# Kernel optimization log

Measured on AMD Instinct MI355X. Metric: run time of the kernel, lower is better.

## Reference

```python
import jax, jax.numpy as jnp
import numpy as np

B, N, C, P, K = 8, 65536, 96, 96, 512


def _ln(x, g, b, eps=1e-5):
    mu = x.mean(axis=-1, keepdims=True)
    var = ((x - mu) ** 2).mean(axis=-1, keepdims=True)
    return (x - mu) * jax.lax.rsqrt(var + eps) * g + b


def setup_inputs():
    key = jax.random.key(0)
    ks = jax.random.split(key, 8)
    inp = {
        "pts_feat": jax.random.normal(ks[0], (B, N, C), jnp.float32),
        "sp_idx": jax.random.randint(ks[1], (B, N), 0, K, jnp.int64),
        "all_xyz": jax.random.normal(ks[2], (B, N, 3), jnp.float32),
        # pts_proj1: Linear(3,P) -> LN -> ReLU -> Linear(P,P) -> LN
        "W1": jax.random.normal(ks[3], (3, P), jnp.float32) / np.sqrt(3.0),
        "b1": jnp.zeros((P,), jnp.float32),
        "g1": jnp.ones((P,), jnp.float32),
        "be1": jnp.zeros((P,), jnp.float32),
        "W2": jax.random.normal(ks[4], (P, P), jnp.float32) / np.sqrt(P),
        "b2": jnp.zeros((P,), jnp.float32),
        "g2": jnp.ones((P,), jnp.float32),
        "be2": jnp.zeros((P,), jnp.float32),
        # pts_proj2: Linear(2P,P) -> LN -> ReLU -> Linear(P,1,no bias) -> Sigmoid
        "W3": jax.random.normal(ks[5], (2 * P, P), jnp.float32) / np.sqrt(2.0 * P),
        "b3": jnp.zeros((P,), jnp.float32),
        "g3": jnp.ones((P,), jnp.float32),
        "be3": jnp.zeros((P,), jnp.float32),
        "W4": jax.random.normal(ks[6], (P, 1), jnp.float32) / np.sqrt(P),
        "num_sp": K,
    }
    return inp


def reference(pts_feat, sp_idx, all_xyz, W1, b1, g1, be1, W2, b2, g2, be2,
              W3, b3, g3, be3, W4, num_sp):
    Bx, Nx, Cx = pts_feat.shape
    S = Bx * num_sp  # total superpoints across batch (uniform K per batch)
    idx = (sp_idx + jnp.arange(Bx, dtype=sp_idx.dtype)[:, None] * num_sp).reshape(-1)
    xyz = all_xyz.reshape(-1, 3)
    feat = pts_feat.reshape(-1, Cx)

    # scatter_norm: unit-sphere normalize per segment
    mn = jax.ops.segment_min(xyz, idx, num_segments=S)
    mx = jax.ops.segment_max(xyz, idx, num_segments=S)
    cnt = jax.ops.segment_sum(jnp.ones((xyz.shape[0],), xyz.dtype), idx, num_segments=S)
    cnt_c = jnp.maximum(cnt, 1.0)
    center = jax.ops.segment_sum(xyz, idx, num_segments=S) / cnt_c[:, None]
    diam = (mx - mn).max(axis=1)
    pts = (xyz - center[idx]) / (diam[idx][:, None] + 0.01)

    # pts_proj1
    h = _ln(pts @ W1 + b1, g1, be1)
    h = jax.nn.relu(h)
    h = _ln(h @ W2 + b2, g2, be2)

    seg = jax.ops.segment_max(h, idx, num_segments=S)  # (S, P)
    cat = jnp.concatenate([h, seg[idx]], axis=-1)      # (B*N, 2P)

    # pts_proj2
    z = _ln(cat @ W3 + b3, g3, be3)
    z = jax.nn.relu(z)
    w = jax.nn.sigmoid(z @ W4) * 2.0                   # (B*N, 1)

    sp_feat = jax.ops.segment_sum(feat * w, idx, num_segments=S) / cnt_c[:, None] + seg
    return sp_feat.reshape(Bx, num_sp, Cx), w.reshape(Bx, Nx, 1)
```

## Files before the change

kernel.cpp:

```cpp
#include <hip/hip_runtime.h>
#include <cstdint>

#define MM 524288
#define NSEG 4096

#define WS_SCNT   0u
#define WS_CURSOR 4096u
#define WS_OFFS   8192u
#define WS_M1     12288u
#define WS_CENTER 12304u
#define WS_DIAM   24592u
#define WS_SEGF   28688u
#define WS_ZSEG   421904u
#define WS_SORTED 815120u
#define WS_SEG16  1339408u
#define WS_WSRT   1601552u
#define WS_H8     2125840u
#define WS_END    (WS_H8 + 25165824u)

typedef __attribute__((ext_vector_type(8))) short short8;
typedef __attribute__((ext_vector_type(4))) float f32x4;

#define WPAD 104

__device__ __forceinline__ unsigned bfr(float x) {
    unsigned u = __float_as_uint(x);
    return (u + 0x7FFFu + ((u >> 16) & 1u)) >> 16;
}
__device__ __forceinline__ float bf2f(unsigned v) {
    return __uint_as_float(v << 16);
}
union U4S8 { uint4 u; short8 s; };

__global__ void __launch_bounds__(256) k0_init(unsigned* __restrict__ ws)
{
    unsigned i = blockIdx.x * 256u + threadIdx.x;
    if (i < 8192u) ws[i] = 0u;
}

__global__ void __launch_bounds__(256) k1_count(
    const int* __restrict__ spidx, unsigned* __restrict__ scnt)
{
    __shared__ unsigned lcnt[512];
    int tid = threadIdx.x;
    for (int j = tid; j < 512; j += 256) lcnt[j] = 0u;
    __syncthreads();
    int base = blockIdx.x * 4096;
    #pragma unroll 4
    for (int it = 0; it < 16; ++it) {
        int p = base + it*256 + tid;
        atomicAdd(&lcnt[spidx[p]], 1u);
    }
    __syncthreads();
    int b = blockIdx.x >> 4;
    for (int j = tid; j < 512; j += 256)
        atomicAdd(&scnt[(b << 9) + j], lcnt[j]);
}

__global__ void __launch_bounds__(1024) k2_scan(
    const unsigned* __restrict__ scnt, unsigned* __restrict__ offs,
    const float* __restrict__ W1, const float* __restrict__ b1, float* __restrict__ m1)
{
    __shared__ unsigned sh[1024];
    int t = threadIdx.x;
    unsigned c0 = scnt[t*4+0], c1 = scnt[t*4+1], c2 = scnt[t*4+2], c3 = scnt[t*4+3];
    unsigned tot = c0 + c1 + c2 + c3;
    sh[t] = tot;
    __syncthreads();
    for (int d = 1; d < 1024; d <<= 1) {
        unsigned v = (t >= d) ? sh[t-d] : 0u;
        __syncthreads();
        sh[t] += v;
        __syncthreads();
    }
    unsigned excl = sh[t] - tot;
    offs[t*4+0] = excl;
    offs[t*4+1] = excl + c0;
    offs[t*4+2] = excl + c0 + c1;
    offs[t*4+3] = excl + c0 + c1 + c2;

    if (t == 0) {
        float Sa=0,Sb=0,Sc=0,Sd=0,Saa=0,Sbb=0,Scc=0,Sdd=0,Sab=0,Sac=0,Sad=0,Sbc=0,Sbd=0,Scd=0;
        #pragma unroll 8
        for (int j = 0; j < 96; ++j) {
            float A = W1[j], B2 = W1[96+j], C2 = W1[192+j], D = b1[j];
            Sa+=A; Sb+=B2; Sc+=C2; Sd+=D;
            Saa=fmaf(A,A,Saa); Sbb=fmaf(B2,B2,Sbb); Scc=fmaf(C2,C2,Scc); Sdd=fmaf(D,D,Sdd);
            Sab=fmaf(A,B2,Sab); Sac=fmaf(A,C2,Sac); Sad=fmaf(A,D,Sad);
            Sbc=fmaf(B2,C2,Sbc); Sbd=fmaf(B2,D,Sbd); Scd=fmaf(C2,D,Scd);
        }
        const float inv = 1.f/96.f;
        float Am=Sa*inv, Bm=Sb*inv, Cm=Sc*inv, Dm=Sd*inv;
        m1[0]=Am; m1[1]=Bm; m1[2]=Cm; m1[3]=Dm;
        m1[4]=Saa*inv-Am*Am; m1[5]=Sbb*inv-Bm*Bm; m1[6]=Scc*inv-Cm*Cm; m1[7]=Sdd*inv-Dm*Dm;
        m1[8]=Sab*inv-Am*Bm; m1[9]=Sac*inv-Am*Cm; m1[10]=Sad*inv-Am*Dm;
        m1[11]=Sbc*inv-Bm*Cm; m1[12]=Sbd*inv-Bm*Dm; m1[13]=Scd*inv-Cm*Dm;
    }
}

__global__ void __launch_bounds__(256) k3_scatter(
    const int* __restrict__ spidx, const unsigned* __restrict__ offs,
    unsigned* __restrict__ cursor, unsigned* __restrict__ sorted,
    unsigned short* __restrict__ seg16)
{
    __shared__ unsigned lcnt[512];
    __shared__ unsigned gbase[512];
    __shared__ unsigned short rank16[4096];
    int tid = threadIdx.x;
    for (int j = tid; j < 512; j += 256) lcnt[j] = 0u;
    __syncthreads();
    int base = blockIdx.x * 4096;
    #pragma unroll 4
    for (int it = 0; it < 16; ++it) {
        int p = base + it*256 + tid;
        unsigned r = atomicAdd(&lcnt[spidx[p]], 1u);
        rank16[it*256 + tid] = (unsigned short)r;
    }
    __syncthreads();
    int b = blockIdx.x >> 4;
    for (int j = tid; j < 512; j += 256)
        gbase[j] = atomicAdd(&cursor[(b << 9) + j], lcnt[j]);
    __syncthreads();
    #pragma unroll 4
    for (int it = 0; it < 16; ++it) {
        int p = base + it*256 + tid;
        int sl = spidx[p];
        int s = (b << 9) + sl;
        unsigned pos = offs[s] + gbase[sl] + (unsigned)rank16[it*256 + tid];
        sorted[pos] = (unsigned)p;
        seg16[pos] = (unsigned short)s;
    }
}

__global__ void __launch_bounds__(128) k3b_stats(
    const float* __restrict__ xyz, const unsigned* __restrict__ sorted,
    const unsigned* __restrict__ offs, const unsigned* __restrict__ scnt,
    float* __restrict__ center, float* __restrict__ diam)
{
    int s = blockIdx.x, tid = threadIdx.x;
    unsigned cnt = scnt[s], off = offs[s];
    float mnx=INFINITY, mny=INFINITY, mnz=INFINITY;
    float mxx=-INFINITY, mxy=-INFINITY, mxz=-INFINITY;
    float smx=0.f, smy=0.f, smz=0.f;
    for (unsigned r = tid; r < cnt; r += 128) {
        unsigned p = sorted[off + r];
        float x = xyz[3*p], y = xyz[3*p+1], z = xyz[3*p+2];
        mnx = fminf(mnx, x); mny = fminf(mny, y); mnz = fminf(mnz, z);
        mxx = fmaxf(mxx, x); mxy = fmaxf(mxy, y); mxz = fmaxf(mxz, z);
        smx += x; smy += y; smz += z;
    }
    #pragma unroll
    for (int m = 1; m < 64; m <<= 1) {
        mnx = fminf(mnx, __shfl_xor(mnx, m)); mny = fminf(mny, __shfl_xor(mny, m));
        mnz = fminf(mnz, __shfl_xor(mnz, m));
        mxx = fmaxf(mxx, __shfl_xor(mxx, m)); mxy = fmaxf(mxy, __shfl_xor(mxy, m));
        mxz = fmaxf(mxz, __shfl_xor(mxz, m));
        smx += __shfl_xor(smx, m); smy += __shfl_xor(smy, m); smz += __shfl_xor(smz, m);
    }
    __shared__ float cw[2][9];
    if ((tid & 63) == 0) {
        int w = tid >> 6;
        cw[w][0]=mnx; cw[w][1]=mny; cw[w][2]=mnz;
        cw[w][3]=mxx; cw[w][4]=mxy; cw[w][5]=mxz;
        cw[w][6]=smx; cw[w][7]=smy; cw[w][8]=smz;
    }
    __syncthreads();
    if (tid == 0) {
        float a0=fminf(cw[0][0],cw[1][0]), a1=fminf(cw[0][1],cw[1][1]), a2=fminf(cw[0][2],cw[1][2]);
        float b0=fmaxf(cw[0][3],cw[1][3]), b1=fmaxf(cw[0][4],cw[1][4]), b2=fmaxf(cw[0][5],cw[1][5]);
        float s0=cw[0][6]+cw[1][6], s1=cw[0][7]+cw[1][7], s2=cw[0][8]+cw[1][8];
        float cc = fmaxf((float)cnt, 1.f);
        center[s*3+0] = s0/cc; center[s*3+1] = s1/cc; center[s*3+2] = s2/cc;
        diam[s] = fmaxf(fmaxf(b0-a0, b1-a1), b2-a2);
    }
}

__global__ void __launch_bounds__(256) kTA(
    const float* __restrict__ xyz,
    const unsigned* __restrict__ sorted,
    const unsigned short* __restrict__ seg16,
    const float* __restrict__ center, const float* __restrict__ diam,
    const float* __restrict__ W1, const float* __restrict__ b1,
    const float* __restrict__ g1, const float* __restrict__ be1,
    const float* __restrict__ m1,
    const float* __restrict__ W2, const float* __restrict__ b2,
    const float* __restrict__ g2, const float* __restrict__ be2,
    uint4* __restrict__ h8)
{
    __shared__ unsigned short wT[96*WPAD];
    __shared__ float pw8[96*8];
    __shared__ float prm[3*96];
    __shared__ float mcl[14];
    int tid = threadIdx.x;
    #pragma unroll 4
    for (int it = 0; it < 36; ++it) {
        int e = it*256 + tid;
        int i = e / 96, j = e - i*96;
        wT[j*WPAD + i] = (unsigned short)bfr(W2[e]);
    }
    if (tid < 96) {
        pw8[tid*8+0] = W1[tid]; pw8[tid*8+1] = W1[96+tid]; pw8[tid*8+2] = W1[192+tid];
        pw8[tid*8+3] = b1[tid]; pw8[tid*8+4] = g1[tid];    pw8[tid*8+5] = be1[tid];
        pw8[tid*8+6] = 0.f;     pw8[tid*8+7] = 0.f;
        prm[tid] = b2[tid]; prm[96+tid] = g2[tid]; prm[192+tid] = be2[tid];
    }
    if (tid < 14) mcl[tid] = m1[tid];
    __syncthreads();

    int lane = tid & 63, w = tid >> 6;
    int pcol = lane & 15, g = lane >> 4;
    size_t slot0 = (size_t)blockIdx.x * 256 + w*64 + pcol;
    const f32x4* pwv = (const f32x4*)pw8;

    #pragma unroll 1
    for (int t = 0; t < 4; ++t) {
        size_t slot = slot0 + (size_t)t * 16;
        unsigned p = sorted[slot];
        int s = seg16[slot];
        float dinv = 1.f / (diam[s] + 0.01f);
        float px = (xyz[3*p+0] - center[3*s+0]) * dinv;
        float py = (xyz[3*p+1] - center[3*s+1]) * dinv;
        float pz = (xyz[3*p+2] - center[3*s+2]) * dinv;

        float mu = fmaf(px, mcl[0], fmaf(py, mcl[1], fmaf(pz, mcl[2], mcl[3])));
        float var = fmaf(px*px, mcl[4], fmaf(py*py, mcl[5], fmaf(pz*pz, mcl[6], mcl[7])));
        var = fmaf(2.f*px*py, mcl[8],  var);
        var = fmaf(2.f*px*pz, mcl[9],  var);
        var = fmaf(2.f*px,    mcl[10], var);
        var = fmaf(2.f*py*pz, mcl[11], var);
        var = fmaf(2.f*py,    mcl[12], var);
        var = fmaf(2.f*pz,    mcl[13], var);
        float rs = rsqrtf(var + 1e-5f);

        f32x4 acc[6];
        #pragma unroll
        for (int nt = 0; nt < 6; ++nt) acc[nt] = (f32x4){0.f,0.f,0.f,0.f};

        #pragma unroll
        for (int ks = 0; ks < 3; ++ks) {
            U4S8 bu;
            unsigned vv[4];
            #pragma unroll
            for (int e2 = 0; e2 < 4; ++e2) {
                int i0 = ks*32 + g*8 + e2*2;
                f32x4 lo0 = pwv[i0*2],     hi0 = pwv[i0*2+1];
                f32x4 lo1 = pwv[(i0+1)*2], hi1 = pwv[(i0+1)*2+1];
                float ta = fmaf(px, lo0[0], fmaf(py, lo0[1], fmaf(pz, lo0[2], lo0[3])));
                ta = fmaxf(fmaf((ta - mu) * rs, hi0[0], hi0[1]), 0.f);
                float tb = fmaf(px, lo1[0], fmaf(py, lo1[1], fmaf(pz, lo1[2], lo1[3])));
                tb = fmaxf(fmaf((tb - mu) * rs, hi1[0], hi1[1]), 0.f);
                vv[e2] = bfr(ta) | (bfr(tb) << 16);
            }
            bu.u.x = vv[0]; bu.u.y = vv[1]; bu.u.z = vv[2]; bu.u.w = vv[3];
            #pragma unroll
            for (int nt = 0; nt < 6; ++nt) {
                const short8 aF = *(const short8*)&wT[(nt*16 + pcol)*WPAD + ks*32 + g*8];
                acc[nt] = __builtin_amdgcn_mfma_f32_16x16x32_bf16(aF, bu.s, acc[nt], 0, 0, 0);
            }
        }

        float sum = 0.f, sq = 0.f;
        #pragma unroll
        for (int nt = 0; nt < 6; ++nt) {
            f32x4 bv = *(const f32x4*)&prm[nt*16 + g*4];
            #pragma unroll
            for (int r = 0; r < 4; ++r) {
                float v = acc[nt][r] + bv[r];
                acc[nt][r] = v;
                sum += v;
                sq = fmaf(v, v, sq);
            }
        }
        sum += __shfl_xor(sum, 16); sum += __shfl_xor(sum, 32);
        sq  += __shfl_xor(sq, 16);  sq  += __shfl_xor(sq, 32);
        float muh = sum * (1.f/96.f);
        float rsh = rsqrtf(sq * (1.f/96.f) - muh*muh + 1e-5f);

        #pragma unroll
        for (int nt = 0; nt < 6; ++nt) {
            f32x4 gv  = *(const f32x4*)&prm[96  + nt*16 + g*4];
            f32x4 bev = *(const f32x4*)&prm[192 + nt*16 + g*4];
            float o0 = fmaf((acc[nt][0]-muh)*rsh, gv[0], bev[0]);
            float o1 = fmaf((acc[nt][1]-muh)*rsh, gv[1], bev[1]);
            float o2 = fmaf((acc[nt][2]-muh)*rsh, gv[2], bev[2]);
            float o3 = fmaf((acc[nt][3]-muh)*rsh, gv[3], bev[3]);
            uint2 st;
            st.x = bfr(o0) | (bfr(o1) << 16);
            st.y = bfr(o2) | (bfr(o3) << 16);
            int j0 = nt*16 + g*4;
            size_t q = (size_t)(nt*2 + (g >> 1));
            *(uint2*)((char*)h8 + (q*MM + slot)*16 + (size_t)(j0 & 7)*2) = st;
        }
    }
}

__global__ void __launch_bounds__(192) kB_seg(
    const uint4* __restrict__ h8,
    const unsigned* __restrict__ offs, const unsigned* __restrict__ scnt,
    const float* __restrict__ W3, const float* __restrict__ b3,
    float* __restrict__ segf, float* __restrict__ zseg)
{
    __shared__ uint4 st[16][13];
    __shared__ float lseg[96];
    int s = blockIdx.x, tid = threadIdx.x;
    unsigned cnt = scnt[s], off = offs[s];
    int r = tid & 15, q = tid >> 4;
    float mx = -INFINITY;
    for (unsigned base = 0; base < cnt; base += 16) {
        uint4 v = make_uint4(0xFF80FF80u, 0xFF80FF80u, 0xFF80FF80u, 0xFF80FF80u);
        if (q < 12 && base + (unsigned)r < cnt)
            v = h8[(size_t)q * MM + off + base + r];
        if (q < 12) st[r][q] = v;
        __syncthreads();
        if (tid < 96) {
            int qj = tid >> 3, ej = tid & 7;
            #pragma unroll
            for (int rr = 0; rr < 16; ++rr) {
                const unsigned short* hp = (const unsigned short*)&st[rr][qj];
                mx = fmaxf(mx, bf2f(hp[ej]));
            }
        }
        __syncthreads();
    }
    if (tid < 96) { segf[(size_t)s*96 + tid] = mx; lseg[tid] = mx; }
    __syncthreads();
    if (tid < 96) {
        float acc = b3[tid];
        #pragma unroll 4
        for (int i = 0; i < 96; ++i)
            acc = fmaf(lseg[i], W3[(size_t)(96+i)*96 + tid], acc);
        zseg[(size_t)s*96 + tid] = acc;
    }
}

__global__ void __launch_bounds__(256) kC_mfma(
    const uint4* __restrict__ h8, const float* __restrict__ zseg,
    const unsigned short* __restrict__ seg16, const unsigned* __restrict__ sorted,
    const float* __restrict__ W3, const float* __restrict__ g3,
    const float* __restrict__ be3, const float* __restrict__ W4,
    float* __restrict__ w_nat, float* __restrict__ w_srt)
{
    __shared__ unsigned short wT[96*WPAD];
    __shared__ float prm[3*96];
    int tid = threadIdx.x;
    #pragma unroll 4
    for (int it = 0; it < 36; ++it) {
        int e = it*256 + tid;
        int i = e / 96, j = e - i*96;
        wT[j*WPAD + i] = (unsigned short)bfr(W3[e]);
    }
    if (tid < 96) { prm[tid] = g3[tid]; prm[96+tid] = be3[tid]; prm[192+tid] = W4[tid]; }
    __syncthreads();

    int lane = tid & 63, w = tid >> 6;
    int pcol = lane & 15, g = lane >> 4;
    size_t slot0 = (size_t)blockIdx.x * 256 + w*64 + pcol;

    uint4 B0 = h8[(size_t)(0*4+g) * MM + slot0];
    uint4 B1 = h8[(size_t)(1*4+g) * MM + slot0];
    uint4 B2q = h8[(size_t)(2*4+g) * MM + slot0];

    #pragma unroll 1
    for (int t = 0; t < 4; ++t) {
        size_t slot = slot0 + (size_t)t * 16;
        uint4 C0 = B0, C1 = B1, C2 = B2q;
        if (t < 3) {
            size_t sn = slot + 16;
            C0 = h8[(size_t)(0*4+g) * MM + sn];
            C1 = h8[(size_t)(1*4+g) * MM + sn];
            C2 = h8[(size_t)(2*4+g) * MM + sn];
        }
        U4S8 u0, u1, u2; u0.u = B0; u1.u = B1; u2.u = B2q;
        short8 bB[3] = { u0.s, u1.s, u2.s };

        f32x4 acc[6];
        #pragma unroll
        for (int nt = 0; nt < 6; ++nt) acc[nt] = (f32x4){0.f,0.f,0.f,0.f};

        #pragma unroll
        for (int ks = 0; ks < 3; ++ks) {
            #pragma unroll
            for (int nt = 0; nt < 6; ++nt) {
                const short8 aF = *(const short8*)&wT[(nt*16 + pcol)*WPAD + ks*32 + g*8];
                acc[nt] = __builtin_amdgcn_mfma_f32_16x16x32_bf16(aF, bB[ks], acc[nt], 0, 0, 0);
            }
        }

        int s = seg16[slot];
        float sum = 0.f, sq = 0.f;
        #pragma unroll
        for (int nt = 0; nt < 6; ++nt) {
            f32x4 zs = *(const f32x4*)&zseg[(size_t)s*96 + nt*16 + g*4];
            #pragma unroll
            for (int r = 0; r < 4; ++r) {
                float v = acc[nt][r] + zs[r];
                acc[nt][r] = v;
                sum += v;
                sq = fmaf(v, v, sq);
            }
        }
        sum += __shfl_xor(sum, 16); sum += __shfl_xor(sum, 32);
        sq  += __shfl_xor(sq, 16);  sq  += __shfl_xor(sq, 32);
        float mu = sum * (1.f/96.f);
        float rs = rsqrtf(sq * (1.f/96.f) - mu*mu + 1e-5f);

        float tt = 0.f;
        #pragma unroll
        for (int nt = 0; nt < 6; ++nt) {
            f32x4 gv  = *(const f32x4*)&prm[nt*16 + g*4];
            f32x4 bev = *(const f32x4*)&prm[96 + nt*16 + g*4];
            f32x4 w4v = *(const f32x4*)&prm[192 + nt*16 + g*4];
            #pragma unroll
            for (int r = 0; r < 4; ++r) {
                float v = fmaxf(fmaf((acc[nt][r]-mu)*rs, gv[r], bev[r]), 0.f);
                tt = fmaf(v, w4v[r], tt);
            }
        }
        tt += __shfl_xor(tt, 16); tt += __shfl_xor(tt, 32);
        if (lane < 16) {
            float wv = 2.f / (1.f + expf(-tt));
            w_srt[slot] = wv;
            w_nat[sorted[slot]] = wv;
        }
        B0 = C0; B1 = C1; B2q = C2;
    }
}

__global__ void __launch_bounds__(128) kD_pool(
    const float* __restrict__ feat, const float* __restrict__ w_srt,
    const unsigned* __restrict__ sorted, const unsigned* __restrict__ offs,
    const unsigned* __restrict__ scnt, const float* __restrict__ segf,
    float* __restrict__ sp_out)
{
    int s = blockIdx.x;
    int c = threadIdx.x;
    unsigned cnt = scnt[s], off = offs[s];
    float acc = 0.f;
    unsigned r = 0;
    for (; r + 8 <= cnt; r += 8) {
        unsigned pp[8]; float ww[8];
        #pragma unroll
        for (int k = 0; k < 8; ++k) {
            pp[k] = sorted[off + r + k];
            ww[k] = w_srt[off + r + k];
        }
        if (c < 96) {
            #pragma unroll
            for (int k = 0; k < 8; ++k)
                acc = fmaf(feat[(size_t)pp[k]*96 + c], ww[k], acc);
        }
    }
    for (; r < cnt; ++r) {
        unsigned p0 = sorted[off + r];
        float w0 = w_srt[off + r];
        if (c < 96) acc = fmaf(feat[(size_t)p0*96 + c], w0, acc);
    }
    if (c < 96) {
        float cc = fmaxf((float)cnt, 1.f);
        sp_out[(size_t)s*96 + c] = acc / cc + segf[(size_t)s*96 + c];
    }
}

extern "C" void kernel_launch(void* const* d_in, const int* in_sizes, int n_in,
                              void* d_out, int out_size, void* d_ws, size_t ws_size,
                              hipStream_t stream)
{
    const float* pts_feat = (const float*)d_in[0];
    const int*   sp_idx   = (const int*)d_in[1];
    const float* xyz      = (const float*)d_in[2];
    const float* W1  = (const float*)d_in[3];
    const float* b1  = (const float*)d_in[4];
    const float* g1  = (const float*)d_in[5];
    const float* be1 = (const float*)d_in[6];
    const float* W2  = (const float*)d_in[7];
    const float* b2  = (const float*)d_in[8];
    const float* g2  = (const float*)d_in[9];
    const float* be2 = (const float*)d_in[10];
    const float* W3  = (const float*)d_in[11];
    const float* b3  = (const float*)d_in[12];
    const float* g3  = (const float*)d_in[13];
    const float* be3 = (const float*)d_in[14];
    const float* W4  = (const float*)d_in[15];

    float* out = (float*)d_out;
    float* sp_out = out;
    float* w_out  = out + (size_t)NSEG * 96;

    if (ws_size < (size_t)WS_END * 4u) return;

    unsigned* ws32   = (unsigned*)d_ws;
    unsigned* scnt   = ws32 + WS_SCNT;
    unsigned* cursor = ws32 + WS_CURSOR;
    unsigned* offs   = ws32 + WS_OFFS;
    float*    m1     = (float*)(ws32 + WS_M1);
    float*    center = (float*)(ws32 + WS_CENTER);
    float*    diam   = (float*)(ws32 + WS_DIAM);
    float*    segf   = (float*)(ws32 + WS_SEGF);
    float*    zseg   = (float*)(ws32 + WS_ZSEG);
    unsigned* sorted = ws32 + WS_SORTED;
    unsigned short* seg16 = (unsigned short*)(ws32 + WS_SEG16);
    float*    w_srt  = (float*)(ws32 + WS_WSRT);
    uint4*    h8     = (uint4*)(ws32 + WS_H8);

    k0_init<<<32, 256, 0, stream>>>(ws32);
    k1_count<<<MM/4096, 256, 0, stream>>>(sp_idx, scnt);
    k2_scan<<<1, 1024, 0, stream>>>(scnt, offs, W1, b1, m1);
    k3_scatter<<<MM/4096, 256, 0, stream>>>(sp_idx, offs, cursor, sorted, seg16);
    k3b_stats<<<NSEG, 128, 0, stream>>>(xyz, sorted, offs, scnt, center, diam);
    kTA<<<MM/256, 256, 0, stream>>>(xyz, sorted, seg16, center, diam,
        W1, b1, g1, be1, m1, W2, b2, g2, be2, h8);
    kB_seg<<<NSEG, 192, 0, stream>>>(h8, offs, scnt, W3, b3, segf, zseg);
    kC_mfma<<<MM/256, 256, 0, stream>>>(h8, zseg, seg16, sorted, W3, g3, be3, W4,
        w_out, w_srt);
    kD_pool<<<NSEG, 128, 0, stream>>>(pts_feat, w_srt, sorted, offs, scnt, segf, sp_out);
}
```

Baseline: 275.9 us.

## Precompute normalized points in stats kernel, double-buffer seg max, deepen pool unroll

k3b_stats now applies the unit-sphere normalization itself and writes the normalized xyz in sorted order as three planar arrays. kTA can then read them with coalesced loads instead of gathering through sorted/seg16 and center/diam. kB_seg double-buffers its shared-memory tile so the next chunk of h8 is loaded while the current one is reduced, dropping one barrier per iteration. kD_pool unrolls its gather to 16 rows with a 4-row tail to keep more loads in flight, at the cost of extra workspace, a second xyz pass in k3b_stats and more registers.

```diff
diff --git a/kernel.cpp b/kernel.cpp
--- a/kernel.cpp
+++ b/kernel.cpp
@@ -8,15 +8,14 @@
 #define WS_CURSOR 4096u
 #define WS_OFFS   8192u
 #define WS_M1     12288u
-#define WS_CENTER 12304u
-#define WS_DIAM   24592u
 #define WS_SEGF   28688u
 #define WS_ZSEG   421904u
 #define WS_SORTED 815120u
 #define WS_SEG16  1339408u
 #define WS_WSRT   1601552u
 #define WS_H8     2125840u
-#define WS_END    (WS_H8 + 25165824u)
+#define WS_PTS    27291664u
+#define WS_END    28864528u
 
 typedef __attribute__((ext_vector_type(8))) short short8;
 typedef __attribute__((ext_vector_type(4))) float f32x4;
@@ -135,7 +134,7 @@
 __global__ void __launch_bounds__(128) k3b_stats(
     const float* __restrict__ xyz, const unsigned* __restrict__ sorted,
     const unsigned* __restrict__ offs, const unsigned* __restrict__ scnt,
-    float* __restrict__ center, float* __restrict__ diam)
+    float* __restrict__ pts)
 {
     int s = blockIdx.x, tid = threadIdx.x;
     unsigned cnt = scnt[s], off = offs[s];
@@ -158,6 +157,7 @@
         smx += __shfl_xor(smx, m); smy += __shfl_xor(smy, m); smz += __shfl_xor(smz, m);
     }
     __shared__ float cw[2][9];
+    __shared__ float cd[4];
     if ((tid & 63) == 0) {
         int w = tid >> 6;
         cw[w][0]=mnx; cw[w][1]=mny; cw[w][2]=mnz;
@@ -170,16 +170,23 @@
         float b0=fmaxf(cw[0][3],cw[1][3]), b1=fmaxf(cw[0][4],cw[1][4]), b2=fmaxf(cw[0][5],cw[1][5]);
         float s0=cw[0][6]+cw[1][6], s1=cw[0][7]+cw[1][7], s2=cw[0][8]+cw[1][8];
         float cc = fmaxf((float)cnt, 1.f);
-        center[s*3+0] = s0/cc; center[s*3+1] = s1/cc; center[s*3+2] = s2/cc;
-        diam[s] = fmaxf(fmaxf(b0-a0, b1-a1), b2-a2);
+        float dm = fmaxf(fmaxf(b0-a0, b1-a1), b2-a2);
+        cd[0] = s0/cc; cd[1] = s1/cc; cd[2] = s2/cc;
+        cd[3] = 1.f / (dm + 0.01f);
+    }
+    __syncthreads();
+    float cx = cd[0], cy = cd[1], cz = cd[2], dinv = cd[3];
+    for (unsigned r = tid; r < cnt; r += 128) {
+        unsigned p = sorted[off + r];
+        unsigned o = off + r;
+        pts[o]              = (xyz[3*p+0] - cx) * dinv;
+        pts[MM + o]         = (xyz[3*p+1] - cy) * dinv;
+        pts[2u*MM + o]      = (xyz[3*p+2] - cz) * dinv;
     }
 }
 
 __global__ void __launch_bounds__(256) kTA(
-    const float* __restrict__ xyz,
-    const unsigned* __restrict__ sorted,
-    const unsigned short* __restrict__ seg16,
-    const float* __restrict__ center, const float* __restrict__ diam,
+    const float* __restrict__ pts,
     const float* __restrict__ W1, const float* __restrict__ b1,
     const float* __restrict__ g1, const float* __restrict__ be1,
     const float* __restrict__ m1,
@@ -215,12 +222,9 @@
     #pragma unroll 1
     for (int t = 0; t < 4; ++t) {
         size_t slot = slot0 + (size_t)t * 16;
-        unsigned p = sorted[slot];
-        int s = seg16[slot];
-        float dinv = 1.f / (diam[s] + 0.01f);
-        float px = (xyz[3*p+0] - center[3*s+0]) * dinv;
-        float py = (xyz[3*p+1] - center[3*s+1]) * dinv;
-        float pz = (xyz[3*p+2] - center[3*s+2]) * dinv;
+        float px = pts[slot];
+        float py = pts[(size_t)MM + slot];
+        float pz = pts[2u*(size_t)MM + slot];
 
         float mu = fmaf(px, mcl[0], fmaf(py, mcl[1], fmaf(pz, mcl[2], mcl[3])));
         float var = fmaf(px*px, mcl[4], fmaf(py*py, mcl[5], fmaf(pz*pz, mcl[6], mcl[7])));
@@ -300,23 +304,33 @@
     const float* __restrict__ W3, const float* __restrict__ b3,
     float* __restrict__ segf, float* __restrict__ zseg)
 {
-    __shared__ uint4 st[16][13];
+    __shared__ uint4 st[2][16][13];
     __shared__ float lseg[96];
     int s = blockIdx.x, tid = threadIdx.x;
     unsigned cnt = scnt[s], off = offs[s];
     int r = tid & 15, q = tid >> 4;
     float mx = -INFINITY;
+
+    if (q < 12) {
+        uint4 v = make_uint4(0xFF80FF80u, 0xFF80FF80u, 0xFF80FF80u, 0xFF80FF80u);
+        if ((unsigned)r < cnt) v = h8[(size_t)q * MM + off + r];
+        st[0][r][q] = v;
+    }
+    __syncthreads();
+
     for (unsigned base = 0; base < cnt; base += 16) {
-        uint4 v = make_uint4(0xFF80FF80u, 0xFF80FF80u, 0xFF80FF80u, 0xFF80FF80u);
-        if (q < 12 && base + (unsigned)r < cnt)
-            v = h8[(size_t)q * MM + off + base + r];
-        if (q < 12) st[r][q] = v;
-        __syncthreads();
+        int cur = (int)((base >> 4) & 1u);
+        unsigned nb = base + 16;
+        if (nb < cnt && q < 12) {
+            uint4 v = make_uint4(0xFF80FF80u, 0xFF80FF80u, 0xFF80FF80u, 0xFF80FF80u);
+            if (nb + (unsigned)r < cnt) v = h8[(size_t)q * MM + off + nb + r];
+            st[cur ^ 1][r][q] = v;
+        }
         if (tid < 96) {
             int qj = tid >> 3, ej = tid & 7;
             #pragma unroll
             for (int rr = 0; rr < 16; ++rr) {
-                const unsigned short* hp = (const unsigned short*)&st[rr][qj];
+                const unsigned short* hp = (const unsigned short*)&st[cur][rr][qj];
                 mx = fmaxf(mx, bf2f(hp[ej]));
             }
         }
@@ -437,16 +451,29 @@
     unsigned cnt = scnt[s], off = offs[s];
     float acc = 0.f;
     unsigned r = 0;
-    for (; r + 8 <= cnt; r += 8) {
-        unsigned pp[8]; float ww[8];
-        #pragma unroll
-        for (int k = 0; k < 8; ++k) {
+    for (; r + 16 <= cnt; r += 16) {
+        unsigned pp[16]; float ww[16];
+        #pragma unroll
+        for (int k = 0; k < 16; ++k) {
             pp[k] = sorted[off + r + k];
             ww[k] = w_srt[off + r + k];
         }
         if (c < 96) {
             #pragma unroll
-            for (int k = 0; k < 8; ++k)
+            for (int k = 0; k < 16; ++k)
+                acc = fmaf(feat[(size_t)pp[k]*96 + c], ww[k], acc);
+        }
+    }
+    for (; r + 4 <= cnt; r += 4) {
+        unsigned pp[4]; float ww[4];
+        #pragma unroll
+        for (int k = 0; k < 4; ++k) {
+            pp[k] = sorted[off + r + k];
+            ww[k] = w_srt[off + r + k];
+        }
+        if (c < 96) {
+            #pragma unroll
+            for (int k = 0; k < 4; ++k)
                 acc = fmaf(feat[(size_t)pp[k]*96 + c], ww[k], acc);
         }
     }
@@ -493,22 +520,21 @@
     unsigned* cursor = ws32 + WS_CURSOR;
     unsigned* offs   = ws32 + WS_OFFS;
     float*    m1     = (float*)(ws32 + WS_M1);
-    float*    center = (float*)(ws32 + WS_CENTER);
-    float*    diam   = (float*)(ws32 + WS_DIAM);
     float*    segf   = (float*)(ws32 + WS_SEGF);
     float*    zseg   = (float*)(ws32 + WS_ZSEG);
     unsigned* sorted = ws32 + WS_SORTED;
     unsigned short* seg16 = (unsigned short*)(ws32 + WS_SEG16);
     float*    w_srt  = (float*)(ws32 + WS_WSRT);
     uint4*    h8     = (uint4*)(ws32 + WS_H8);
+    float*    pts    = (float*)(ws32 + WS_PTS);
 
     k0_init<<<32, 256, 0, stream>>>(ws32);
     k1_count<<<MM/4096, 256, 0, stream>>>(sp_idx, scnt);
     k2_scan<<<1, 1024, 0, stream>>>(scnt, offs, W1, b1, m1);
     k3_scatter<<<MM/4096, 256, 0, stream>>>(sp_idx, offs, cursor, sorted, seg16);
-    k3b_stats<<<NSEG, 128, 0, stream>>>(xyz, sorted, offs, scnt, center, diam);
-    kTA<<<MM/256, 256, 0, stream>>>(xyz, sorted, seg16, center, diam,
-        W1, b1, g1, be1, m1, W2, b2, g2, be2, h8);
+    k3b_stats<<<NSEG, 128, 0, stream>>>(xyz, sorted, offs, scnt, pts);
+    kTA<<<MM/256, 256, 0, stream>>>(pts, W1, b1, g1, be1, m1,
+        W2, b2, g2, be2, h8);
     kB_seg<<<NSEG, 192, 0, stream>>>(h8, offs, scnt, W3, b3, segf, zseg);
     kC_mfma<<<MM/256, 256, 0, stream>>>(h8, zseg, seg16, sorted, W3, g3, be3, W4,
         w_out, w_srt);
```

Measured after the change: 264.5 us, median of 2. -4.2%, faster.
